# Kernel optimization log

Measured on AMD Instinct MI355X. Metric: run time of the kernel, lower is better.

Reference implementation:

```python
import jax, jax.numpy as jnp
import numpy as np

B, G, D, H, L, MLP = 64, 512, 384, 6, 12, 4
DH = D // H
MASK_RATIO = 0.6
KEEP_RATIO = 0.1
PAD_VAL = -1.0
START_VAL = 1.0
POS_HID = 128
NEG = -1e9


def setup_inputs() -> dict:
    key = jax.random.key(0)
    ks = jax.random.split(key, 24)
    s = 0.02
    inp = {
        "x": jax.random.normal(ks[0], (B, G, D), jnp.float32),
        "center_points": jax.random.normal(ks[1], (B, G, 3), jnp.float32),
        "mask_noise": jax.random.uniform(ks[2], (B, G), jnp.float32),
        # pos embedder MLP: 3 -> 128 -> D
        "pos_w1": jax.random.normal(ks[3], (3, POS_HID), jnp.float32) * s,
        "pos_b1": jnp.zeros((POS_HID,), jnp.float32),
        "pos_w2": jax.random.normal(ks[4], (POS_HID, D), jnp.float32) * s,
        "pos_b2": jnp.zeros((D,), jnp.float32),
        # stacked per-layer transformer params
        "ln1_w": jnp.ones((L, D), jnp.float32),
        "ln1_b": jnp.zeros((L, D), jnp.float32),
        "qkv_w": jax.random.normal(ks[5], (L, D, 3 * D), jnp.float32) * s,
        "qkv_b": jnp.zeros((L, 3 * D), jnp.float32),
        "proj_w": jax.random.normal(ks[6], (L, D, D), jnp.float32) * s,
        "proj_b": jnp.zeros((L, D), jnp.float32),
        "ln2_w": jnp.ones((L, D), jnp.float32),
        "ln2_b": jnp.zeros((L, D), jnp.float32),
        "fc1_w": jax.random.normal(ks[7], (L, D, MLP * D), jnp.float32) * s,
        "fc1_b": jnp.zeros((L, MLP * D), jnp.float32),
        "fc2_w": jax.random.normal(ks[8], (L, MLP * D, D), jnp.float32) * s,
        "fc2_b": jnp.zeros((L, D), jnp.float32),
        # final LayerNorm
        "norm_w": jnp.ones((D,), jnp.float32),
        "norm_b": jnp.zeros((D,), jnp.float32),
    }
    return inp


def _layer_norm(h, w, b, eps=1e-5):
    mu = jnp.mean(h, axis=-1, keepdims=True)
    var = jnp.mean(jnp.square(h - mu), axis=-1, keepdims=True)
    return (h - mu) * jax.lax.rsqrt(var + eps) * w + b


def _random_mask(center, noise):
    # padding tokens: all coords equal PAD_VAL
    pad = jnp.all(center == PAD_VAL, axis=-1)                      # [B, G] bool
    if MASK_RATIO == 0:
        return jnp.zeros(pad.shape, bool), pad
    n = (G - jnp.sum(pad.astype(jnp.int32), axis=-1))              # non-padding count
    k = (n.astype(jnp.float32) * KEEP_RATIO).astype(jnp.int32)     # kept-first tokens
    m = ((n - k).astype(jnp.float32) * MASK_RATIO).astype(jnp.int32)
    M = jnp.max(m)
    j = jnp.arange(G)[None, :]
    # shuffle region [k, n): pick m random slots (uniform subset via rank of noise)
    region = (j >= k[:, None]) & (j < n[:, None])
    u = jnp.where(region, noise, jnp.inf)
    rank = jnp.argsort(jnp.argsort(u, axis=-1), axis=-1)
    shuf = (rank < m[:, None]) & region
    # tail of ones: positions [n, n + M - m)
    tail = (j >= n[:, None]) & (j < (n + M - m)[:, None])
    return shuf | tail, pad


def _attention(h, qw, qb, pw, pb, bias):
    qkv = (h @ qw + qb).reshape(B, G, 3, H, DH).transpose(2, 0, 3, 1, 4)
    q, k, v = qkv[0], qkv[1], qkv[2]                               # [B, H, G, DH]
    s = jnp.einsum('bhqd,bhkd->bhqk', q, k) * (DH ** -0.5) + bias
    a = jax.nn.softmax(s, axis=-1)
    o = jnp.einsum('bhqk,bhkd->bhqd', a, v).transpose(0, 2, 1, 3).reshape(B, G, D)
    return o @ pw + pb


def _forward(x, center_points, mask_noise,
             pos_w1, pos_b1, pos_w2, pos_b2,
             ln1_w, ln1_b, qkv_w, qkv_b, proj_w, proj_b,
             ln2_w, ln2_b, fc1_w, fc1_b, fc2_w, fc2_b,
             norm_w, norm_b):
    # shift right + start token
    start = jnp.full((B, 1, D), START_VAL, x.dtype)
    x = jnp.concatenate([start, x[:, :-1, :]], axis=1)
    # positional embedding of shifted centers + start-token pos
    pos = jax.nn.gelu(center_points[:, :-1, :] @ pos_w1 + pos_b1, approximate=False) @ pos_w2 + pos_b2
    pos = jnp.concatenate([jnp.full((B, 1, D), START_VAL, x.dtype), pos], axis=1)
    # causal | (random column mask & ~eye) attention mask
    triu = jnp.triu(jnp.ones((G, G), bool), 1)
    rand_mask, pad = _random_mask(center_points, mask_noise)
    eye = jnp.eye(G, dtype=bool)
    attn_mask = triu[None, :, :] | (rand_mask[:, None, :] & ~eye[None, :, :])   # [B, G, G]
    bias = jnp.where(attn_mask | pad[:, None, :], NEG, 0.0)[:, None, :, :]      # [B,1,G,G]

    def block(h, p):
        l1w, l1b, qw, qb, pw, pb, l2w, l2b, f1w, f1b, f2w, f2b = p
        h = h + pos
        h = h + _attention(_layer_norm(h, l1w, l1b), qw, qb, pw, pb, bias)
        h = h + (jax.nn.gelu(_layer_norm(h, l2w, l2b) @ f1w + f1b, approximate=False) @ f2w + f2b)
        return h, None

    x, _ = jax.lax.scan(block, x, (ln1_w, ln1_b, qkv_w, qkv_b, proj_w, proj_b,
                                   ln2_w, ln2_b, fc1_w, fc1_b, fc2_w, fc2_b))
    x = _layer_norm(x, norm_w, norm_b)
    return x, pad, attn_mask


def reference(x, center_points, mask_noise,
              pos_w1, pos_b1, pos_w2, pos_b2,
              ln1_w, ln1_b, qkv_w, qkv_b, proj_w, proj_b,
              ln2_w, ln2_b, fc1_w, fc1_b, fc2_w, fc2_b,
              norm_w, norm_b):
    out, pad, attn_mask = _forward(x, center_points, mask_noise,
                                   pos_w1, pos_b1, pos_w2, pos_b2,
                                   ln1_w, ln1_b, qkv_w, qkv_b, proj_w, proj_b,
                                   ln2_w, ln2_b, fc1_w, fc1_b, fc2_w, fc2_b,
                                   norm_w, norm_b)
    # torch repeat_interleave over heads -> [B*H, G, G]
    return out, pad, jnp.repeat(attn_mask, H, axis=0)
```

## Files before the change

kernel.cpp:

```cpp
#include <hip/hip_runtime.h>
#include <math.h>

typedef _Float16 f16;
typedef f16 f16x8 __attribute__((ext_vector_type(8)));
typedef float f32x4 __attribute__((ext_vector_type(4)));

#define NB 64
#define NG 512
#define ND 384
#define NH 6
#define NL 12
#define NDH 64
#define BG (NB * NG)
#define BGD (BG * ND)

#define OFF_WQKV   0
#define OFF_WPROJ  2654208
#define OFF_WFC1   3538944
#define OFF_WFC2   7077888
#define OFF_FLAGS  10616832
#define OFF_NKM    10625024
#define OFF_MMAX   10625216
#define OFF_POS    10625280
#define OFF_HID    23208192
#define OFF_Y      27402496
#define OFF_YBIG   33693952
#define OFF_QB     58859776
#define OFF_KB     65151232
#define OFF_VT     71442688
#define OFF_OB     77734144
#define OFF_W2T    84025600

typedef __attribute__((address_space(3))) void lds_t;
typedef const __attribute__((address_space(1))) void gmem_t;
__device__ __forceinline__ void gload16(const void* g, void* l)
{
    __builtin_amdgcn_global_load_lds((gmem_t*)g, (lds_t*)l, 16, 0, 0);
}

__global__ __launch_bounds__(256)
void transpose_kernel(const float* __restrict__ src, f16* __restrict__ dst,
                      int K, int N)
{
    __shared__ float tile[32][33];
    const int l = blockIdx.z;
    const float* S = src + (size_t)l * K * N;
    f16* D = dst + (size_t)l * K * N;
    const int n0 = blockIdx.x * 32, k0 = blockIdx.y * 32;
    const int tx = threadIdx.x, ty = threadIdx.y;
#pragma unroll
    for (int i = 0; i < 32; i += 8)
        tile[ty + i][tx] = S[(size_t)(k0 + ty + i) * N + n0 + tx];
    __syncthreads();
#pragma unroll
    for (int i = 0; i < 32; i += 8)
        D[(size_t)(n0 + ty + i) * K + k0 + tx] = (f16)tile[tx][ty + i];
}

__global__ __launch_bounds__(256)
void dpos_a(const float* cen, const float* w1, const float* b1, f16* hid)
{
    const int idx = blockIdx.x * 256 + threadIdx.x;
    if (idx >= BG * 128) return;
    const int t = idx >> 7, k = idx & 127;
    const int g = t & (NG - 1);
    if (g == 0) { hid[idx] = (f16)0.f; return; }
    const float* c = cen + (size_t)(t - 1) * 3;
    const float hv = c[0] * w1[k] + c[1] * w1[128 + k] + c[2] * w1[256 + k] + b1[k];
    hid[idx] = (f16)(0.5f * hv * (1.0f + erff(hv * 0.70710678118654752f)));
}

__global__ __launch_bounds__(384)
void pos_fix(float* pos)
{
    const int b = blockIdx.x;
    pos[((size_t)b * NG) * ND + threadIdx.x] = 1.0f;
}

__global__ __launch_bounds__(512)
void dmask_a(const float* cen, float* pad_out, int* nkm)
{
    const int b = blockIdx.x, j = threadIdx.x;
    const float* c = cen + ((size_t)b * NG + j) * 3;
    const bool pad = (c[0] == -1.f) && (c[1] == -1.f) && (c[2] == -1.f);
    pad_out[b * NG + j] = pad ? 1.f : 0.f;
    if (j == 0) {
        int cnt = 0;
        for (int i = 0; i < NG; i++) {
            const float* ci = cen + ((size_t)b * NG + i) * 3;
            cnt += (ci[0] == -1.f && ci[1] == -1.f && ci[2] == -1.f) ? 1 : 0;
        }
        const int n = NG - cnt;
        const int k = (int)((float)n * 0.1f);
        const int m = (int)((float)(n - k) * 0.6f);
        nkm[b * 3] = n; nkm[b * 3 + 1] = k; nkm[b * 3 + 2] = m;
    }
}

__global__ void dmask_m(const int* nkm, int* Mmax)
{
    if (threadIdx.x == 0 && blockIdx.x == 0) {
        int M = 0;
        for (int b = 0; b < NB; b++) M = max(M, nkm[b * 3 + 2]);
        *Mmax = M;
    }
}

__global__ __launch_bounds__(512)
void dmask_b(const float* cen, const float* noi, const int* nkm,
             const int* Mmax, unsigned char* flags)
{
    const int b = blockIdx.x, j = threadIdx.x;
    const int n = nkm[b * 3], k = nkm[b * 3 + 1], m = nkm[b * 3 + 2];
    const int M = *Mmax;
    const float nz = noi[b * NG + j];
    const bool inreg = (j >= k) && (j < n);
    bool shuf = false;
    if (inreg) {
        int cnt = 0;
        for (int i = 0; i < NG; i++) {
            if (i < k || i >= n) continue;
            const float ui = noi[b * NG + i];
            cnt += (ui < nz) || (ui == nz && i < j);
        }
        shuf = cnt < m;
    }
    const float* c = cen + ((size_t)b * NG + j) * 3;
    const bool pad = (c[0] == -1.f) && (c[1] == -1.f) && (c[2] == -1.f);
    const bool tail = (j >= n) && (j < n + M - m);
    flags[b * NG + j] = (unsigned char)(((shuf | tail) ? 1 : 0) | (pad ? 2 : 0));
}

__global__ __launch_bounds__(512)
void flags_rep_kernel(const unsigned char* flags, float* mo)
{
    const int bq = blockIdx.x;
    const int b = bq >> 9, q = bq & (NG - 1);
    const int j = threadIdx.x;
    mo[(((size_t)(b * NH) * NG + q) * NG) + j] = (float)flags[b * NG + j];
}

__global__ __launch_bounds__(512)
void mask_out_kernel(float* mo)
{
    const int bq = blockIdx.x;
    const int b = bq >> 9, q = bq & (NG - 1);
    const int j = threadIdx.x;
    const unsigned char f =
        (unsigned char)mo[(((size_t)(b * NH) * NG + q) * NG) + j];
    const float val = ((q < j) || ((f & 1) && (q != j))) ? 1.0f : 0.0f;
#pragma unroll
    for (int h = 0; h < NH; h++)
        mo[(((size_t)(b * NH + h) * NG + q) * NG) + j] = val;
}

__global__ __launch_bounds__(256)
void h0_kernel(const float* x, float* h)
{
    const size_t i = (size_t)blockIdx.x * 256 + threadIdx.x;
    const int g = (int)((i / ND) & (NG - 1));
    const float xv = x[(g == 0) ? i : (i - ND)];
    h[i] = (g == 0) ? 1.0f : xv;
}

template<int MODE>
__global__ __launch_bounds__(64)
void lnb_kernel(float* __restrict__ h, const float* __restrict__ pos,
                const float* __restrict__ w, const float* __restrict__ bb,
                f16* __restrict__ y16, float* __restrict__ y32)
{
    __shared__ float red[64];
    const int t = blockIdx.x;
    const int lane = threadIdx.x;
    const size_t base = (size_t)t * ND + lane;
    float v[6];
    float s = 0.f;
#pragma unroll
    for (int i = 0; i < 6; i++) {
        float xv = h[base + i * 64];
        if constexpr (MODE == 0) xv += pos[base + i * 64];
        v[i] = xv; s += xv;
    }
    if constexpr (MODE == 0) {
#pragma unroll
        for (int i = 0; i < 6; i++) h[base + i * 64] = v[i];
    }
    red[lane] = s;
    __syncthreads();
    for (int st = 32; st > 0; st >>= 1) {
        if (lane < st) red[lane] += red[lane + st];
        __syncthreads();
    }
    const float mu = red[0] * (1.f / ND);
    float vs = 0.f;
#pragma unroll
    for (int i = 0; i < 6; i++) { const float d = v[i] - mu; vs += d * d; }
    __syncthreads();
    red[lane] = vs;
    __syncthreads();
    for (int st = 32; st > 0; st >>= 1) {
        if (lane < st) red[lane] += red[lane + st];
        __syncthreads();
    }
    const float rstd = rsqrtf(red[0] * (1.f / ND) + 1e-5f);
#pragma unroll
    for (int i = 0; i < 6; i++) {
        const float o = (v[i] - mu) * rstd * w[lane + i * 64] + bb[lane + i * 64];
        if constexpr (MODE == 2) y32[base + i * 64] = o;
        else                     y16[base + i * 64] = (f16)o;
    }
}

template<int MODE>
__global__ __launch_bounds__(256)
void gemm_kernel(const f16* __restrict__ A, const f16* __restrict__ Bt,
                 const float* __restrict__ bias, int K, int NT,
                 float* __restrict__ hbuf, f16* __restrict__ out16,
                 f16* __restrict__ Qo, f16* __restrict__ Ko, f16* __restrict__ Vo)
{
    __shared__ f16 sA[128 * 64];
    __shared__ f16 sB[128 * 64];
    const int tid = threadIdx.x;
    const int w = tid >> 6, lane = tid & 63;
    const int lr = lane & 15, lg = lane >> 4;
    const int wm = w >> 1, wn = w & 1;
    const int N = NT * 128;

    const int nwg = gridDim.x;
    const int chunk = nwg >> 3;
    const int flat = (blockIdx.x & 7) * chunk + (blockIdx.x >> 3);
    const int m0 = (flat / NT) * 128;
    const int n0 = (flat % NT) * 128;

    f32x4 acc[4][4];
#pragma unroll
    for (int mf = 0; mf < 4; mf++)
#pragma unroll
        for (int nf = 0; nf < 4; nf++)
            acc[mf][nf] = (f32x4){0.f, 0.f, 0.f, 0.f};

    const int srow0 = w * 8 + (lane >> 3);
    const int scolB = (lane & 7) * 16;

    for (int k0 = 0; k0 < K; k0 += 64) {
        __syncthreads();
#pragma unroll
        for (int i = 0; i < 4; i++) {
            const int row = i * 32 + srow0;
            const int colB = scolB ^ ((row & 7) << 4);
            const char* ga = (const char*)(A + (size_t)(m0 + row) * K + k0) + colB;
            const char* gb = (const char*)(Bt + (size_t)(n0 + row) * K + k0) + colB;
            gload16(ga, (char*)sA + row * 128 + scolB);
            gload16(gb, (char*)sB + row * 128 + scolB);
        }
        __syncthreads();
#pragma unroll
        for (int kk = 0; kk < 64; kk += 32) {
            f16x8 af[4], bf[4];
#pragma unroll
            for (int mf = 0; mf < 4; mf++) {
                const int r = wm * 64 + mf * 16 + lr;
                const int cb = ((kk + lg * 8) * 2) ^ ((r & 7) << 4);
                af[mf] = *(const f16x8*)((const char*)sA + r * 128 + cb);
            }
#pragma unroll
            for (int nf = 0; nf < 4; nf++) {
                const int r = wn * 64 + nf * 16 + lr;
                const int cb = ((kk + lg * 8) * 2) ^ ((r & 7) << 4);
                bf[nf] = *(const f16x8*)((const char*)sB + r * 128 + cb);
            }
#pragma unroll
            for (int mf = 0; mf < 4; mf++)
#pragma unroll
                for (int nf = 0; nf < 4; nf++)
                    acc[mf][nf] = __builtin_amdgcn_mfma_f32_16x16x32_f16(
                        af[mf], bf[nf], acc[mf][nf], 0, 0, 0);
        }
    }

#pragma unroll
    for (int mf = 0; mf < 4; mf++) {
#pragma unroll
        for (int nf = 0; nf < 4; nf++) {
            const int n_g = n0 + wn * 64 + nf * 16 + lr;
            const float bv = bias[n_g];
#pragma unroll
            for (int r = 0; r < 4; r++) {
                const int m_g = m0 + wm * 64 + mf * 16 + lg * 4 + r;
                const float v = acc[mf][nf][r] + bv;
                if constexpr (MODE == 1) {
                    hbuf[(size_t)m_g * N + n_g] += v;
                } else if constexpr (MODE == 2) {
                    const float ge = 0.5f * v * (1.0f + erff(v * 0.70710678118654752f));
                    out16[(size_t)m_g * N + n_g] = (f16)ge;
                } else if constexpr (MODE == 3) {
                    hbuf[(size_t)m_g * N + n_g] = v;
                } else {
                    const int which = n_g / ND;
                    const int rem = n_g - which * ND;
                    const int hh = rem >> 6, dh = rem & 63;
                    const int bb2 = m_g >> 9, gg = m_g & (NG - 1);
                    if (which == 0)
                        Qo[((size_t)(bb2 * NH + hh) * NG + gg) * NDH + dh] = (f16)v;
                    else if (which == 1)
                        Ko[((size_t)(bb2 * NH + hh) * NG + gg) * NDH + dh] = (f16)v;
                    else
                        Vo[((size_t)(bb2 * NH + hh) * NDH + dh) * NG + gg] = (f16)v;
                }
            }
        }
    }
}

__global__ __launch_bounds__(256)
void attn_kernel(const f16* __restrict__ Q, const f16* __restrict__ Kt,
                 const f16* __restrict__ V, const unsigned char* __restrict__ flags,
                 f16* __restrict__ O)
{
    __shared__ f16 sQ[64][72];
    __shared__ f16 sK[64][72];
    __shared__ f16 sV[64][72];
    __shared__ f16 sP[4][16][72];
    const int tid = threadIdx.x;
    const int w = tid >> 6, lane = tid & 63;
    const int lr = lane & 15, lg = lane >> 4;
    const int q0 = blockIdx.x * 64;
    const int bh = blockIdx.y;
    const int b = bh / NH, hh = bh - b * NH;
    const f16* Qg = Q + ((size_t)bh * NG + q0) * NDH;
    const f16* Kg = Kt + (size_t)bh * NG * NDH;
    const f16* Vg = V + (size_t)bh * NDH * NG;
    const unsigned char* fl = flags + b * NG;

#pragma unroll
    for (int i = 0; i < 2; i++) {
        const int c = tid + i * 256;
        const int r = c >> 3, cc = (c & 7) * 8;
        *(f16x8*)&sQ[r][cc] = *(const f16x8*)(Qg + r * NDH + cc);
    }
    __syncthreads();
    f16x8 aq[2];
    aq[0] = *(const f16x8*)&sQ[w * 16 + lr][lg * 8];
    aq[1] = *(const f16x8*)&sQ[w * 16 + lr][32 + lg * 8];

    float m_run[4], l_run[4];
    f32x4 o[4];
#pragma unroll
    for (int r = 0; r < 4; r++) { m_run[r] = -INFINITY; l_run[r] = 0.f; }
#pragma unroll
    for (int nf = 0; nf < 4; nf++) o[nf] = (f32x4){0.f, 0.f, 0.f, 0.f};

    const int ntile = blockIdx.x + 1;
    for (int jt = 0; jt < ntile; jt++) {
        const int j0 = jt * 64;
        __syncthreads();
#pragma unroll
        for (int i = 0; i < 2; i++) {
            const int c = tid + i * 256;
            const int r = c >> 3, cc = (c & 7) * 8;
            *(f16x8*)&sK[r][cc] = *(const f16x8*)(Kg + (size_t)(j0 + r) * NDH + cc);
            *(f16x8*)&sV[r][cc] = *(const f16x8*)(Vg + (size_t)r * NG + j0 + cc);
        }
        __syncthreads();

        f32x4 s[4];
#pragma unroll
        for (int nf = 0; nf < 4; nf++) s[nf] = (f32x4){0.f, 0.f, 0.f, 0.f};
#pragma unroll
        for (int kf = 0; kf < 2; kf++) {
#pragma unroll
            for (int nf = 0; nf < 4; nf++) {
                f16x8 bk = *(const f16x8*)&sK[nf * 16 + lr][kf * 32 + lg * 8];
                s[nf] = __builtin_amdgcn_mfma_f32_16x16x32_f16(aq[kf], bk, s[nf], 0, 0, 0);
            }
        }
#pragma unroll
        for (int nf = 0; nf < 4; nf++) {
            const int j_g = j0 + nf * 16 + lr;
            const unsigned char f = fl[j_g];
#pragma unroll
            for (int r = 0; r < 4; r++) {
                const int q_g = q0 + w * 16 + lg * 4 + r;
                const bool masked = (q_g < j_g) || (f & 2) || ((f & 1) && (j_g != q_g));
                s[nf][r] = s[nf][r] * 0.125f + (masked ? -1e9f : 0.f);
            }
        }
#pragma unroll
        for (int r = 0; r < 4; r++) {
            float mx = fmaxf(fmaxf(s[0][r], s[1][r]), fmaxf(s[2][r], s[3][r]));
#pragma unroll
            for (int off = 1; off < 16; off <<= 1) mx = fmaxf(mx, __shfl_xor(mx, off));
            const float nm = fmaxf(m_run[r], mx);
            const float sc = __expf(m_run[r] - nm);
            m_run[r] = nm;
            l_run[r] *= sc;
#pragma unroll
            for (int nf = 0; nf < 4; nf++) o[nf][r] *= sc;
            float ls = 0.f;
#pragma unroll
            for (int nf = 0; nf < 4; nf++) {
                const float p = __expf(s[nf][r] - nm);
                ls += p;
                sP[w][lg * 4 + r][nf * 16 + lr] = (f16)p;
            }
            l_run[r] += ls;
        }
#pragma unroll
        for (int kf = 0; kf < 2; kf++) {
            f16x8 ap = *(const f16x8*)&sP[w][lr][kf * 32 + lg * 8];
#pragma unroll
            for (int nf = 0; nf < 4; nf++) {
                f16x8 bv = *(const f16x8*)&sV[nf * 16 + lr][kf * 32 + lg * 8];
                o[nf] = __builtin_amdgcn_mfma_f32_16x16x32_f16(ap, bv, o[nf], 0, 0, 0);
            }
        }
    }

    float inv[4];
#pragma unroll
    for (int r = 0; r < 4; r++) {
        float l = l_run[r];
#pragma unroll
        for (int off = 1; off < 16; off <<= 1) l += __shfl_xor(l, off);
        inv[r] = 1.f / l;
    }
#pragma unroll
    for (int nf = 0; nf < 4; nf++) {
#pragma unroll
        for (int r = 0; r < 4; r++) {
            const int q_g = q0 + w * 16 + lg * 4 + r;
            const int dh = nf * 16 + lr;
            O[((size_t)(b * NG + q_g)) * ND + hh * NDH + dh] = (f16)(o[nf][r] * inv[r]);
        }
    }
}

extern "C" void kernel_launch(void* const* d_in, const int* in_sizes, int n_in,
                              void* d_out, int out_size, void* d_ws, size_t ws_size,
                              hipStream_t stream)
{
    (void)d_ws; (void)ws_size;

    static const int exp_sizes[21] = {
        12582912, 98304, 32768,
        384, 128, 49152, 384,
        4608, 4608,
        5308416, 13824,
        1769472, 4608,
        4608, 4608,
        7077888, 18432,
        7077888, 4608,
        384, 384
    };
    if (n_in != 21 || out_size != 113278976) return;
    for (int i = 0; i < 21; i++) if (in_sizes[i] != exp_sizes[i]) return;

    const float* x    = (const float*)d_in[0];
    const float* cen  = (const float*)d_in[1];
    const float* noi  = (const float*)d_in[2];
    const float* pw1  = (const float*)d_in[3];
    const float* pb1  = (const float*)d_in[4];
    const float* pw2  = (const float*)d_in[5];
    const float* pb2  = (const float*)d_in[6];
    const float* ln1w = (const float*)d_in[7];
    const float* ln1b = (const float*)d_in[8];
    const float* qkvw = (const float*)d_in[9];
    const float* qkvb = (const float*)d_in[10];
    const float* projw= (const float*)d_in[11];
    const float* projb= (const float*)d_in[12];
    const float* ln2w = (const float*)d_in[13];
    const float* ln2b = (const float*)d_in[14];
    const float* fc1w = (const float*)d_in[15];
    const float* fc1b = (const float*)d_in[16];
    const float* fc2w = (const float*)d_in[17];
    const float* fc2b = (const float*)d_in[18];
    const float* nw   = (const float*)d_in[19];
    const float* nb   = (const float*)d_in[20];

    float* out0    = (float*)d_out;
    float* pad_out = out0 + BGD;
    float* R       = pad_out + BG;

    float* Hb   = out0;
    f16* WqkvT  = (f16*)(R + OFF_WQKV);
    f16* WprojT = (f16*)(R + OFF_WPROJ);
    f16* Wfc1T  = (f16*)(R + OFF_WFC1);
    f16* Wfc2T  = (f16*)(R + OFF_WFC2);
    unsigned char* flags = (unsigned char*)(R + OFF_FLAGS);
    int* nkm  = (int*)(R + OFF_NKM);
    int* Mmax = (int*)(R + OFF_MMAX);
    float* POS = R + OFF_POS;
    f16* HID   = (f16*)(R + OFF_HID);
    f16* Y     = (f16*)(R + OFF_Y);
    f16* Ybig  = (f16*)(R + OFF_YBIG);
    f16* Qb    = (f16*)(R + OFF_QB);
    f16* Kb    = (f16*)(R + OFF_KB);
    f16* Vt    = (f16*)(R + OFF_VT);
    f16* Ob    = (f16*)(R + OFF_OB);
    f16* W2T   = (f16*)(R + OFF_W2T);

    dim3 tb(32, 8);
    transpose_kernel<<<dim3(36, 12, NL), tb, 0, stream>>>(qkvw, WqkvT, 384, 1152);
    transpose_kernel<<<dim3(12, 12, NL), tb, 0, stream>>>(projw, WprojT, 384, 384);
    transpose_kernel<<<dim3(48, 12, NL), tb, 0, stream>>>(fc1w, Wfc1T, 384, 1536);
    transpose_kernel<<<dim3(12, 48, NL), tb, 0, stream>>>(fc2w, Wfc2T, 1536, 384);
    transpose_kernel<<<dim3(12, 4, 1),  tb, 0, stream>>>(pw2, W2T, 128, 384);

    dmask_a<<<NB, 512, 0, stream>>>(cen, pad_out, nkm);
    dmask_m<<<1, 64, 0, stream>>>(nkm, Mmax);
    dmask_b<<<NB, 512, 0, stream>>>(cen, noi, nkm, Mmax, flags);
    dpos_a<<<BG * 128 / 256, 256, 0, stream>>>(cen, pw1, pb1, HID);
    gemm_kernel<3><<<768, 256, 0, stream>>>(HID, W2T, pb2, 128, 3,
                                            POS, nullptr, nullptr, nullptr, nullptr);
    pos_fix<<<NB, 384, 0, stream>>>(POS);
    h0_kernel<<<BGD / 256, 256, 0, stream>>>(x, Hb);

    for (int l = 0; l < NL; l++) {
        lnb_kernel<0><<<BG, 64, 0, stream>>>(Hb, POS, ln1w + l * ND, ln1b + l * ND, Y, nullptr);
        gemm_kernel<0><<<2304, 256, 0, stream>>>(Y, WqkvT + (size_t)l * 442368,
                                                 qkvb + l * 1152, 384, 9,
                                                 nullptr, nullptr, Qb, Kb, Vt);
        attn_kernel<<<dim3(8, NB * NH), 256, 0, stream>>>(Qb, Kb, Vt, flags, Ob);
        gemm_kernel<1><<<768, 256, 0, stream>>>(Ob, WprojT + (size_t)l * 147456,
                                                projb + l * ND, 384, 3,
                                                Hb, nullptr, nullptr, nullptr, nullptr);
        lnb_kernel<1><<<BG, 64, 0, stream>>>(Hb, nullptr, ln2w + l * ND, ln2b + l * ND, Y, nullptr);
        gemm_kernel<2><<<3072, 256, 0, stream>>>(Y, Wfc1T + (size_t)l * 589824,
                                                 fc1b + l * 1536, 384, 12,
                                                 nullptr, Ybig, nullptr, nullptr, nullptr);
        gemm_kernel<1><<<768, 256, 0, stream>>>(Ybig, Wfc2T + (size_t)l * 589824,
                                                fc2b + l * ND, 1536, 3,
                                                Hb, nullptr, nullptr, nullptr, nullptr);
    }

    lnb_kernel<2><<<BG, 64, 0, stream>>>(Hb, nullptr, nw, nb, nullptr, out0);
    flags_rep_kernel<<<BG, 512, 0, stream>>>(flags, R);
    mask_out_kernel<<<BG, 512, 0, stream>>>(R);
}
```

Measured before the change: 5.252 ms.

## Compact unmasked keys per batch so attention skips masked key tiles

Builds a per-batch index of keys that are neither padded nor random-masked, and has the QKV GEMM scatter K and V into compacted 256-wide buffers. Attention then loops only over compacted key tiles, covering the unmasked keys before each query block, and adds the diagonal self-key term for masked queries in a final correction step. This removes work on masked key tiles at the cost of extra scatter writes, extra kernels, and a hard cap of 256 unmasked keys per batch.

```diff
diff --git a/kernel.cpp b/kernel.cpp
--- a/kernel.cpp
+++ b/kernel.cpp
@@ -30,6 +30,12 @@
 #define OFF_VT     71442688
 #define OFF_OB     77734144
 #define OFF_W2T    84025600
+#define OFF_KC     84050176
+#define OFF_VC     87195904
+#define OFF_UB     90341632
+#define OFF_IDX    90349824
+#define OFF_CNTQ   90366208
+#define OFF_TOT    90366720
 
 typedef __attribute__((address_space(3))) void lds_t;
 typedef const __attribute__((address_space(1))) void gmem_t;
@@ -132,6 +138,45 @@
 }
 
 __global__ __launch_bounds__(512)
+void cidx_kernel(const unsigned char* flags, unsigned short* Ub,
+                 unsigned short* idxt, int* cntq, int* tot)
+{
+    __shared__ unsigned char sf[NG];
+    __shared__ int stot;
+    const int b = blockIdx.x, j = threadIdx.x;
+    sf[j] = flags[b * NG + j] & 3;
+    __syncthreads();
+    int cnt = 0;
+    for (int i = 0; i < j; i++) cnt += (sf[i] == 0) ? 1 : 0;
+    const bool um = (sf[j] == 0);
+    if (um && cnt < 256) {
+        Ub[b * 256 + cnt] = (unsigned short)j;
+        idxt[b * NG + j] = (unsigned short)cnt;
+    } else {
+        idxt[b * NG + j] = 0xFFFF;
+    }
+    if ((j & 63) == 63) cntq[b * 8 + (j >> 6)] = cnt + (um ? 1 : 0);
+    if (j == NG - 1) stot = cnt + (um ? 1 : 0);
+    __syncthreads();
+    if (j < 256 && j >= stot) Ub[b * 256 + j] = 0xFFFF;
+    if (j == 0) tot[b] = stot;
+}
+
+__global__ __launch_bounds__(256)
+void cpad_kernel(const int* tot, f16* Kc, f16* Vc)
+{
+    const int bh = blockIdx.x;
+    const int b = bh / NH;
+    const int t0 = tot[b];
+    const int n = (256 - t0) * NDH;
+    for (int e = threadIdx.x; e < n; e += 256) {
+        const int i = t0 + e / NDH, d = e % NDH;
+        Kc[((size_t)bh * 256 + i) * NDH + d] = (f16)0.f;
+        Vc[((size_t)bh * NDH + d) * 256 + i] = (f16)0.f;
+    }
+}
+
+__global__ __launch_bounds__(512)
 void flags_rep_kernel(const unsigned char* flags, float* mo)
 {
     const int bq = blockIdx.x;
@@ -216,7 +261,9 @@
 void gemm_kernel(const f16* __restrict__ A, const f16* __restrict__ Bt,
                  const float* __restrict__ bias, int K, int NT,
                  float* __restrict__ hbuf, f16* __restrict__ out16,
-                 f16* __restrict__ Qo, f16* __restrict__ Ko, f16* __restrict__ Vo)
+                 f16* __restrict__ Qo, f16* __restrict__ Ko, f16* __restrict__ Vo,
+                 const unsigned short* __restrict__ idxt,
+                 f16* __restrict__ Kc, f16* __restrict__ Vc)
 {
     __shared__ f16 sA[128 * 64];
     __shared__ f16 sB[128 * 64];
@@ -300,12 +347,20 @@
                     const int rem = n_g - which * ND;
                     const int hh = rem >> 6, dh = rem & 63;
                     const int bb2 = m_g >> 9, gg = m_g & (NG - 1);
-                    if (which == 0)
+                    if (which == 0) {
                         Qo[((size_t)(bb2 * NH + hh) * NG + gg) * NDH + dh] = (f16)v;
-                    else if (which == 1)
-                        Ko[((size_t)(bb2 * NH + hh) * NG + gg) * NDH + dh] = (f16)v;
-                    else
-                        Vo[((size_t)(bb2 * NH + hh) * NDH + dh) * NG + gg] = (f16)v;
+                    } else {
+                        const unsigned short ix = idxt[bb2 * NG + gg];
+                        if (which == 1) {
+                            Ko[((size_t)(bb2 * NH + hh) * NG + gg) * NDH + dh] = (f16)v;
+                            if (ix != 0xFFFF)
+                                Kc[((size_t)(bb2 * NH + hh) * 256 + ix) * NDH + dh] = (f16)v;
+                        } else {
+                            Vo[((size_t)(bb2 * NH + hh) * NDH + dh) * NG + gg] = (f16)v;
+                            if (ix != 0xFFFF)
+                                Vc[((size_t)(bb2 * NH + hh) * NDH + dh) * 256 + ix] = (f16)v;
+                        }
+                    }
                 }
             }
         }
@@ -313,14 +368,21 @@
 }
 
 __global__ __launch_bounds__(256)
-void attn_kernel(const f16* __restrict__ Q, const f16* __restrict__ Kt,
-                 const f16* __restrict__ V, const unsigned char* __restrict__ flags,
+void attn_kernel(const f16* __restrict__ Q, const f16* __restrict__ Kfull,
+                 const f16* __restrict__ Vfull,
+                 const f16* __restrict__ Kc, const f16* __restrict__ Vc,
+                 const unsigned short* __restrict__ Ub,
+                 const int* __restrict__ cntq,
+                 const unsigned char* __restrict__ flags,
                  f16* __restrict__ O)
 {
     __shared__ f16 sQ[64][72];
     __shared__ f16 sK[64][72];
     __shared__ f16 sV[64][72];
     __shared__ f16 sP[4][16][72];
+    __shared__ unsigned short sU[256];
+    __shared__ float sPart[64][4];
+    __shared__ float sdg[64];
     const int tid = threadIdx.x;
     const int w = tid >> 6, lane = tid & 63;
     const int lr = lane & 15, lg = lane >> 4;
@@ -328,8 +390,8 @@
     const int bh = blockIdx.y;
     const int b = bh / NH, hh = bh - b * NH;
     const f16* Qg = Q + ((size_t)bh * NG + q0) * NDH;
-    const f16* Kg = Kt + (size_t)bh * NG * NDH;
-    const f16* Vg = V + (size_t)bh * NDH * NG;
+    const f16* Kcg = Kc + (size_t)bh * 256 * NDH;
+    const f16* Vcg = Vc + (size_t)bh * NDH * 256;
     const unsigned char* fl = flags + b * NG;
 
 #pragma unroll
@@ -338,7 +400,23 @@
         const int r = c >> 3, cc = (c & 7) * 8;
         *(f16x8*)&sQ[r][cc] = *(const f16x8*)(Qg + r * NDH + cc);
     }
-    __syncthreads();
+    sU[tid] = Ub[b * 256 + tid];
+    __syncthreads();
+
+    {
+        const int r2 = tid >> 2, part = tid & 3;
+        const f16* kr = Kfull + ((size_t)bh * NG + q0 + r2) * NDH + part * 16;
+        float a = 0.f;
+#pragma unroll
+        for (int d = 0; d < 16; d++)
+            a += (float)sQ[r2][part * 16 + d] * (float)kr[d];
+        sPart[r2][part] = a;
+    }
+    __syncthreads();
+    if (tid < 64)
+        sdg[tid] = (sPart[tid][0] + sPart[tid][1] + sPart[tid][2] + sPart[tid][3]) * 0.125f;
+    __syncthreads();
+
     f16x8 aq[2];
     aq[0] = *(const f16x8*)&sQ[w * 16 + lr][lg * 8];
     aq[1] = *(const f16x8*)&sQ[w * 16 + lr][32 + lg * 8];
@@ -350,7 +428,7 @@
 #pragma unroll
     for (int nf = 0; nf < 4; nf++) o[nf] = (f32x4){0.f, 0.f, 0.f, 0.f};
 
-    const int ntile = blockIdx.x + 1;
+    const int ntile = (cntq[b * 8 + blockIdx.x] + 63) >> 6;
     for (int jt = 0; jt < ntile; jt++) {
         const int j0 = jt * 64;
         __syncthreads();
@@ -358,8 +436,8 @@
         for (int i = 0; i < 2; i++) {
             const int c = tid + i * 256;
             const int r = c >> 3, cc = (c & 7) * 8;
-            *(f16x8*)&sK[r][cc] = *(const f16x8*)(Kg + (size_t)(j0 + r) * NDH + cc);
-            *(f16x8*)&sV[r][cc] = *(const f16x8*)(Vg + (size_t)r * NG + j0 + cc);
+            *(f16x8*)&sK[r][cc] = *(const f16x8*)(Kcg + (size_t)(j0 + r) * NDH + cc);
+            *(f16x8*)&sV[r][cc] = *(const f16x8*)(Vcg + (size_t)r * 256 + j0 + cc);
         }
         __syncthreads();
 
@@ -376,13 +454,11 @@
         }
 #pragma unroll
         for (int nf = 0; nf < 4; nf++) {
-            const int j_g = j0 + nf * 16 + lr;
-            const unsigned char f = fl[j_g];
+            const unsigned int Uv = sU[j0 + nf * 16 + lr];
 #pragma unroll
             for (int r = 0; r < 4; r++) {
-                const int q_g = q0 + w * 16 + lg * 4 + r;
-                const bool masked = (q_g < j_g) || (f & 2) || ((f & 1) && (j_g != q_g));
-                s[nf][r] = s[nf][r] * 0.125f + (masked ? -1e9f : 0.f);
+                const unsigned int q_g = q0 + w * 16 + lg * 4 + r;
+                s[nf][r] = s[nf][r] * 0.125f + ((Uv > q_g) ? -1e9f : 0.f);
             }
         }
 #pragma unroll
@@ -416,13 +492,24 @@
         }
     }
 
-    float inv[4];
 #pragma unroll
     for (int r = 0; r < 4; r++) {
         float l = l_run[r];
 #pragma unroll
         for (int off = 1; off < 16; off <<= 1) l += __shfl_xor(l, off);
-        inv[r] = 1.f / l;
+        const int rr = w * 16 + lg * 4 + r;
+        const int q_g = q0 + rr;
+        const float sd = ((fl[q_g] & 3) == 1) ? sdg[rr] : -1e30f;
+        const float nm = fmaxf(m_run[r], sd);
+        const float sc = __expf(m_run[r] - nm);
+        const float pd = __expf(sd - nm);
+        const float inv = 1.f / (l * sc + pd);
+#pragma unroll
+        for (int nf = 0; nf < 4; nf++) {
+            const int dh = nf * 16 + lr;
+            const float vd = (float)Vfull[((size_t)bh * NDH + dh) * NG + q_g];
+            o[nf][r] = (o[nf][r] * sc + pd * vd) * inv;
+        }
     }
 #pragma unroll
     for (int nf = 0; nf < 4; nf++) {
@@ -430,7 +517,7 @@
         for (int r = 0; r < 4; r++) {
             const int q_g = q0 + w * 16 + lg * 4 + r;
             const int dh = nf * 16 + lr;
-            O[((size_t)(b * NG + q_g)) * ND + hh * NDH + dh] = (f16)(o[nf][r] * inv[r]);
+            O[((size_t)(b * NG + q_g)) * ND + hh * NDH + dh] = (f16)o[nf][r];
         }
     }
 }
@@ -498,6 +585,12 @@
     f16* Vt    = (f16*)(R + OFF_VT);
     f16* Ob    = (f16*)(R + OFF_OB);
     f16* W2T   = (f16*)(R + OFF_W2T);
+    f16* Kc    = (f16*)(R + OFF_KC);
+    f16* Vc    = (f16*)(R + OFF_VC);
+    unsigned short* Ub   = (unsigned short*)(R + OFF_UB);
+    unsigned short* idxt = (unsigned short*)(R + OFF_IDX);
+    int* cntq = (int*)(R + OFF_CNTQ);
+    int* tot  = (int*)(R + OFF_TOT);
 
     dim3 tb(32, 8);
     transpose_kernel<<<dim3(36, 12, NL), tb, 0, stream>>>(qkvw, WqkvT, 384, 1152);
@@ -509,9 +602,12 @@
     dmask_a<<<NB, 512, 0, stream>>>(cen, pad_out, nkm);
     dmask_m<<<1, 64, 0, stream>>>(nkm, Mmax);
     dmask_b<<<NB, 512, 0, stream>>>(cen, noi, nkm, Mmax, flags);
+    cidx_kernel<<<NB, 512, 0, stream>>>(flags, Ub, idxt, cntq, tot);
+    cpad_kernel<<<NB * NH, 256, 0, stream>>>(tot, Kc, Vc);
     dpos_a<<<BG * 128 / 256, 256, 0, stream>>>(cen, pw1, pb1, HID);
     gemm_kernel<3><<<768, 256, 0, stream>>>(HID, W2T, pb2, 128, 3,
-                                            POS, nullptr, nullptr, nullptr, nullptr);
+                                            POS, nullptr, nullptr, nullptr, nullptr,
+                                            nullptr, nullptr, nullptr);
     pos_fix<<<NB, 384, 0, stream>>>(POS);
     h0_kernel<<<BGD / 256, 256, 0, stream>>>(x, Hb);
 
@@ -519,18 +615,23 @@
         lnb_kernel<0><<<BG, 64, 0, stream>>>(Hb, POS, ln1w + l * ND, ln1b + l * ND, Y, nullptr);
         gemm_kernel<0><<<2304, 256, 0, stream>>>(Y, WqkvT + (size_t)l * 442368,
                                                  qkvb + l * 1152, 384, 9,
-                                                 nullptr, nullptr, Qb, Kb, Vt);
-        attn_kernel<<<dim3(8, NB * NH), 256, 0, stream>>>(Qb, Kb, Vt, flags, Ob);
+                                                 nullptr, nullptr, Qb, Kb, Vt,
+                                                 idxt, Kc, Vc);
+        attn_kernel<<<dim3(8, NB * NH), 256, 0, stream>>>(Qb, Kb, Vt, Kc, Vc,
+                                                          Ub, cntq, flags, Ob);
         gemm_kernel<1><<<768, 256, 0, stream>>>(Ob, WprojT + (size_t)l * 147456,
                                                 projb + l * ND, 384, 3,
-                                                Hb, nullptr, nullptr, nullptr, nullptr);
+                                                Hb, nullptr, nullptr, nullptr, nullptr,
+                                                nullptr, nullptr, nullptr);
         lnb_kernel<1><<<BG, 64, 0, stream>>>(Hb, nullptr, ln2w + l * ND, ln2b + l * ND, Y, nullptr);
         gemm_kernel<2><<<3072, 256, 0, stream>>>(Y, Wfc1T + (size_t)l * 589824,
                                                  fc1b + l * 1536, 384, 12,
-                                                 nullptr, Ybig, nullptr, nullptr, nullptr);
+                                                 nullptr, Ybig, nullptr, nullptr, nullptr,
+                                                 nullptr, nullptr, nullptr);
         gemm_kernel<1><<<768, 256, 0, stream>>>(Ybig, Wfc2T + (size_t)l * 589824,
                                                 fc2b + l * ND, 1536, 3,
-                                                Hb, nullptr, nullptr, nullptr, nullptr);
+                                                Hb, nullptr, nullptr, nullptr, nullptr,
+                                                nullptr, nullptr, nullptr);
     }
 
     lnb_kernel<2><<<BG, 64, 0, stream>>>(Hb, nullptr, nw, nb, nullptr, out0);
```

After: 5.548 ms. +5.6%, slower.

## Process 128 queries per attention block and pack four rows per layernorm block

Applied to the files above, without the earlier changes.

The attention kernel now covers 128 query rows per block, held as two 64-row halves. Each K/V tile loaded into shared memory is reused across both halves, and the upper half skips the last tile, which is fully masked for it. This cuts K/V global loads and halves the block count, at the cost of more registers and fewer blocks to hide latency and balance the causal work. Separately, the layernorm kernels pack four token rows into a 256-thread block so each block does more work and fewer tiny 64-thread blocks are launched.

```diff
diff --git a/kernel.cpp b/kernel.cpp
--- a/kernel.cpp
+++ b/kernel.cpp
@@ -164,14 +164,15 @@
 }
 
 template<int MODE>
-__global__ __launch_bounds__(64)
+__global__ __launch_bounds__(256)
 void lnb_kernel(float* __restrict__ h, const float* __restrict__ pos,
                 const float* __restrict__ w, const float* __restrict__ bb,
                 f16* __restrict__ y16, float* __restrict__ y32)
 {
-    __shared__ float red[64];
-    const int t = blockIdx.x;
-    const int lane = threadIdx.x;
+    __shared__ float red[4][64];
+    const int wid = threadIdx.x >> 6;
+    const int lane = threadIdx.x & 63;
+    const int t = blockIdx.x * 4 + wid;
     const size_t base = (size_t)t * ND + lane;
     float v[6];
     float s = 0.f;
@@ -185,24 +186,24 @@
 #pragma unroll
         for (int i = 0; i < 6; i++) h[base + i * 64] = v[i];
     }
-    red[lane] = s;
+    red[wid][lane] = s;
     __syncthreads();
     for (int st = 32; st > 0; st >>= 1) {
-        if (lane < st) red[lane] += red[lane + st];
+        if (lane < st) red[wid][lane] += red[wid][lane + st];
         __syncthreads();
     }
-    const float mu = red[0] * (1.f / ND);
+    const float mu = red[wid][0] * (1.f / ND);
     float vs = 0.f;
 #pragma unroll
     for (int i = 0; i < 6; i++) { const float d = v[i] - mu; vs += d * d; }
     __syncthreads();
-    red[lane] = vs;
+    red[wid][lane] = vs;
     __syncthreads();
     for (int st = 32; st > 0; st >>= 1) {
-        if (lane < st) red[lane] += red[lane + st];
+        if (lane < st) red[wid][lane] += red[wid][lane + st];
         __syncthreads();
     }
-    const float rstd = rsqrtf(red[0] * (1.f / ND) + 1e-5f);
+    const float rstd = rsqrtf(red[wid][0] * (1.f / ND) + 1e-5f);
 #pragma unroll
     for (int i = 0; i < 6; i++) {
         const float o = (v[i] - mu) * rstd * w[lane + i * 64] + bb[lane + i * 64];
@@ -317,14 +318,14 @@
                  const f16* __restrict__ V, const unsigned char* __restrict__ flags,
                  f16* __restrict__ O)
 {
-    __shared__ f16 sQ[64][72];
+    __shared__ f16 sQ[128][72];
     __shared__ f16 sK[64][72];
     __shared__ f16 sV[64][72];
     __shared__ f16 sP[4][16][72];
     const int tid = threadIdx.x;
     const int w = tid >> 6, lane = tid & 63;
     const int lr = lane & 15, lg = lane >> 4;
-    const int q0 = blockIdx.x * 64;
+    const int q0 = blockIdx.x * 128;
     const int bh = blockIdx.y;
     const int b = bh / NH, hh = bh - b * NH;
     const f16* Qg = Q + ((size_t)bh * NG + q0) * NDH;
@@ -333,24 +334,30 @@
     const unsigned char* fl = flags + b * NG;
 
 #pragma unroll
-    for (int i = 0; i < 2; i++) {
+    for (int i = 0; i < 4; i++) {
         const int c = tid + i * 256;
         const int r = c >> 3, cc = (c & 7) * 8;
         *(f16x8*)&sQ[r][cc] = *(const f16x8*)(Qg + r * NDH + cc);
     }
     __syncthreads();
-    f16x8 aq[2];
-    aq[0] = *(const f16x8*)&sQ[w * 16 + lr][lg * 8];
-    aq[1] = *(const f16x8*)&sQ[w * 16 + lr][32 + lg * 8];
-
-    float m_run[4], l_run[4];
-    f32x4 o[4];
-#pragma unroll
-    for (int r = 0; r < 4; r++) { m_run[r] = -INFINITY; l_run[r] = 0.f; }
-#pragma unroll
-    for (int nf = 0; nf < 4; nf++) o[nf] = (f32x4){0.f, 0.f, 0.f, 0.f};
-
-    const int ntile = blockIdx.x + 1;
+    f16x8 aq[2][2];
+#pragma unroll
+    for (int hf = 0; hf < 2; hf++) {
+        aq[hf][0] = *(const f16x8*)&sQ[hf * 64 + w * 16 + lr][lg * 8];
+        aq[hf][1] = *(const f16x8*)&sQ[hf * 64 + w * 16 + lr][32 + lg * 8];
+    }
+
+    float m_run[2][4], l_run[2][4];
+    f32x4 o[2][4];
+#pragma unroll
+    for (int hf = 0; hf < 2; hf++)
+#pragma unroll
+        for (int r = 0; r < 4; r++) {
+            m_run[hf][r] = -INFINITY; l_run[hf][r] = 0.f;
+            o[hf][r] = (f32x4){0.f, 0.f, 0.f, 0.f};
+        }
+
+    const int ntile = 2 * blockIdx.x + 2;
     for (int jt = 0; jt < ntile; jt++) {
         const int j0 = jt * 64;
         __syncthreads();
@@ -363,74 +370,81 @@
         }
         __syncthreads();
 
-        f32x4 s[4];
-#pragma unroll
-        for (int nf = 0; nf < 4; nf++) s[nf] = (f32x4){0.f, 0.f, 0.f, 0.f};
-#pragma unroll
-        for (int kf = 0; kf < 2; kf++) {
+#pragma unroll
+        for (int hf = 0; hf < 2; hf++) {
+            if (jt >= ntile - 1 + hf) continue;
+            f32x4 s[4];
+#pragma unroll
+            for (int nf = 0; nf < 4; nf++) s[nf] = (f32x4){0.f, 0.f, 0.f, 0.f};
+#pragma unroll
+            for (int kf = 0; kf < 2; kf++) {
+#pragma unroll
+                for (int nf = 0; nf < 4; nf++) {
+                    f16x8 bk = *(const f16x8*)&sK[nf * 16 + lr][kf * 32 + lg * 8];
+                    s[nf] = __builtin_amdgcn_mfma_f32_16x16x32_f16(aq[hf][kf], bk, s[nf], 0, 0, 0);
+                }
+            }
 #pragma unroll
             for (int nf = 0; nf < 4; nf++) {
-                f16x8 bk = *(const f16x8*)&sK[nf * 16 + lr][kf * 32 + lg * 8];
-                s[nf] = __builtin_amdgcn_mfma_f32_16x16x32_f16(aq[kf], bk, s[nf], 0, 0, 0);
-            }
+                const int j_g = j0 + nf * 16 + lr;
+                const unsigned char f = fl[j_g];
+#pragma unroll
+                for (int r = 0; r < 4; r++) {
+                    const int q_g = q0 + hf * 64 + w * 16 + lg * 4 + r;
+                    const bool masked = (q_g < j_g) || (f & 2) || ((f & 1) && (j_g != q_g));
+                    s[nf][r] = s[nf][r] * 0.125f + (masked ? -1e9f : 0.f);
+                }
+            }
+#pragma unroll
+            for (int r = 0; r < 4; r++) {
+                float mx = fmaxf(fmaxf(s[0][r], s[1][r]), fmaxf(s[2][r], s[3][r]));
+#pragma unroll
+                for (int off = 1; off < 16; off <<= 1) mx = fmaxf(mx, __shfl_xor(mx, off));
+                const float nm = fmaxf(m_run[hf][r], mx);
+                const float sc = __expf(m_run[hf][r] - nm);
+                m_run[hf][r] = nm;
+                l_run[hf][r] *= sc;
+#pragma unroll
+                for (int nf = 0; nf < 4; nf++) o[hf][nf][r] *= sc;
+                float ls = 0.f;
+#pragma unroll
+                for (int nf = 0; nf < 4; nf++) {
+                    const float p = __expf(s[nf][r] - nm);
+                    ls += p;
+                    sP[w][lg * 4 + r][nf * 16 + lr] = (f16)p;
+                }
+                l_run[hf][r] += ls;
+            }
+#pragma unroll
+            for (int kf = 0; kf < 2; kf++) {
+                f16x8 ap = *(const f16x8*)&sP[w][lr][kf * 32 + lg * 8];
+#pragma unroll
+                for (int nf = 0; nf < 4; nf++) {
+                    f16x8 bv = *(const f16x8*)&sV[nf * 16 + lr][kf * 32 + lg * 8];
+                    o[hf][nf] = __builtin_amdgcn_mfma_f32_16x16x32_f16(ap, bv, o[hf][nf], 0, 0, 0);
+                }
+            }
+        }
+    }
+
+#pragma unroll
+    for (int hf = 0; hf < 2; hf++) {
+        float inv[4];
+#pragma unroll
+        for (int r = 0; r < 4; r++) {
+            float l = l_run[hf][r];
+#pragma unroll
+            for (int off = 1; off < 16; off <<= 1) l += __shfl_xor(l, off);
+            inv[r] = 1.f / l;
         }
 #pragma unroll
         for (int nf = 0; nf < 4; nf++) {
-            const int j_g = j0 + nf * 16 + lr;
-            const unsigned char f = fl[j_g];
 #pragma unroll
             for (int r = 0; r < 4; r++) {
-                const int q_g = q0 + w * 16 + lg * 4 + r;
-                const bool masked = (q_g < j_g) || (f & 2) || ((f & 1) && (j_g != q_g));
-                s[nf][r] = s[nf][r] * 0.125f + (masked ? -1e9f : 0.f);
-            }
-        }
-#pragma unroll
-        for (int r = 0; r < 4; r++) {
-            float mx = fmaxf(fmaxf(s[0][r], s[1][r]), fmaxf(s[2][r], s[3][r]));
-#pragma unroll
-            for (int off = 1; off < 16; off <<= 1) mx = fmaxf(mx, __shfl_xor(mx, off));
-            const float nm = fmaxf(m_run[r], mx);
-            const float sc = __expf(m_run[r] - nm);
-            m_run[r] = nm;
-            l_run[r] *= sc;
-#pragma unroll
-            for (int nf = 0; nf < 4; nf++) o[nf][r] *= sc;
-            float ls = 0.f;
-#pragma unroll
-            for (int nf = 0; nf < 4; nf++) {
-                const float p = __expf(s[nf][r] - nm);
-                ls += p;
-                sP[w][lg * 4 + r][nf * 16 + lr] = (f16)p;
-            }
-            l_run[r] += ls;
-        }
-#pragma unroll
-        for (int kf = 0; kf < 2; kf++) {
-            f16x8 ap = *(const f16x8*)&sP[w][lr][kf * 32 + lg * 8];
-#pragma unroll
-            for (int nf = 0; nf < 4; nf++) {
-                f16x8 bv = *(const f16x8*)&sV[nf * 16 + lr][kf * 32 + lg * 8];
-                o[nf] = __builtin_amdgcn_mfma_f32_16x16x32_f16(ap, bv, o[nf], 0, 0, 0);
-            }
-        }
-    }
-
-    float inv[4];
-#pragma unroll
-    for (int r = 0; r < 4; r++) {
-        float l = l_run[r];
-#pragma unroll
-        for (int off = 1; off < 16; off <<= 1) l += __shfl_xor(l, off);
-        inv[r] = 1.f / l;
-    }
-#pragma unroll
-    for (int nf = 0; nf < 4; nf++) {
-#pragma unroll
-        for (int r = 0; r < 4; r++) {
-            const int q_g = q0 + w * 16 + lg * 4 + r;
-            const int dh = nf * 16 + lr;
-            O[((size_t)(b * NG + q_g)) * ND + hh * NDH + dh] = (f16)(o[nf][r] * inv[r]);
+                const int q_g = q0 + hf * 64 + w * 16 + lg * 4 + r;
+                const int dh = nf * 16 + lr;
+                O[((size_t)(b * NG + q_g)) * ND + hh * NDH + dh] = (f16)(o[hf][nf][r] * inv[r]);
+            }
         }
     }
 }
@@ -516,15 +530,15 @@
     h0_kernel<<<BGD / 256, 256, 0, stream>>>(x, Hb);
 
     for (int l = 0; l < NL; l++) {
-        lnb_kernel<0><<<BG, 64, 0, stream>>>(Hb, POS, ln1w + l * ND, ln1b + l * ND, Y, nullptr);
+        lnb_kernel<0><<<BG / 4, 256, 0, stream>>>(Hb, POS, ln1w + l * ND, ln1b + l * ND, Y, nullptr);
         gemm_kernel<0><<<2304, 256, 0, stream>>>(Y, WqkvT + (size_t)l * 442368,
                                                  qkvb + l * 1152, 384, 9,
                                                  nullptr, nullptr, Qb, Kb, Vt);
-        attn_kernel<<<dim3(8, NB * NH), 256, 0, stream>>>(Qb, Kb, Vt, flags, Ob);
+        attn_kernel<<<dim3(4, NB * NH), 256, 0, stream>>>(Qb, Kb, Vt, flags, Ob);
         gemm_kernel<1><<<768, 256, 0, stream>>>(Ob, WprojT + (size_t)l * 147456,
                                                 projb + l * ND, 384, 3,
                                                 Hb, nullptr, nullptr, nullptr, nullptr);
-        lnb_kernel<1><<<BG, 64, 0, stream>>>(Hb, nullptr, ln2w + l * ND, ln2b + l * ND, Y, nullptr);
+        lnb_kernel<1><<<BG / 4, 256, 0, stream>>>(Hb, nullptr, ln2w + l * ND, ln2b + l * ND, Y, nullptr);
         gemm_kernel<2><<<3072, 256, 0, stream>>>(Y, Wfc1T + (size_t)l * 589824,
                                                  fc1b + l * 1536, 384, 12,
                                                  nullptr, Ybig, nullptr, nullptr, nullptr);
@@ -533,7 +547,7 @@
                                                 Hb, nullptr, nullptr, nullptr, nullptr);
     }
 
-    lnb_kernel<2><<<BG, 64, 0, stream>>>(Hb, nullptr, nw, nb, nullptr, out0);
+    lnb_kernel<2><<<BG / 4, 256, 0, stream>>>(Hb, nullptr, nw, nb, nullptr, out0);
     flags_rep_kernel<<<BG, 512, 0, stream>>>(flags, R);
     mask_out_kernel<<<BG, 512, 0, stream>>>(R);
 }
```

New measurement: 5.288 ms. Within noise of the previous version (+0.7%).
